# Optimization experiments

Hardware: AMD Instinct MI355X
Metric: run time of the kernel (lower is better)

Reference implementation:

```python
import jax, jax.numpy as jnp
import numpy as np

N = 50000      # nodes
E = 500000     # edges
H = 128        # hidden_channels
P = 1024       # number of (src,dst) link pairs: z==1 and z==2 counts
L = 3          # num_layers
MAXZ = 1000


def setup_inputs() -> dict:
    key = jax.random.key(0)
    ks = jax.random.split(key, 16)
    # z: P src nodes (label 1), P dst nodes (label 2), rest random labels >= 3
    z = jnp.concatenate([
        jnp.ones((P,), jnp.int32),
        jnp.full((P,), 2, jnp.int32),
        jax.random.randint(ks[0], (N - 2 * P,), 3, MAXZ, dtype=jnp.int32),
    ])
    edge_index = jax.random.randint(ks[1], (2, E), 0, N, dtype=jnp.int32)
    batch = jnp.zeros((N,), jnp.int32)  # unused in executed branch
    s = 1.0 / np.sqrt(H)
    z_table = jax.random.normal(ks[2], (MAXZ, H), jnp.float32) * 0.1
    conv_Wl = jax.random.normal(ks[3], (L, H, H), jnp.float32) * s
    conv_bl = jax.random.normal(ks[4], (L, H), jnp.float32) * 0.01
    conv_Wr = jax.random.normal(ks[5], (L, H, H), jnp.float32) * s
    W0 = jax.random.normal(ks[6], (H, H), jnp.float32) * s
    b0 = jax.random.normal(ks[7], (H,), jnp.float32) * 0.01
    W1 = jax.random.normal(ks[8], (H, H), jnp.float32) * s
    b1 = jax.random.normal(ks[9], (H,), jnp.float32) * 0.01
    W2 = jax.random.normal(ks[10], (1, H), jnp.float32) * s
    b2 = jax.random.normal(ks[11], (1,), jnp.float32) * 0.01
    return dict(z=z, edge_index=edge_index, batch=batch, z_table=z_table,
                conv_Wl=conv_Wl, conv_bl=conv_bl, conv_Wr=conv_Wr,
                W0=W0, b0=b0, W1=W1, b1=b1, W2=W2, b2=b2)


def _sage_conv(x, Wl, bl, Wr, src, dst):
    # x: [2, N, H]; mean-aggregate neighbor messages then linear (PyG SAGEConv)
    msgs = x[:, src, :]  # [2, E, H] gather
    agg = jax.vmap(lambda m: jax.ops.segment_sum(m, dst, num_segments=N))(msgs)
    deg = jax.ops.segment_sum(jnp.ones((dst.shape[0],), x.dtype), dst, num_segments=N)
    agg = agg / jnp.maximum(deg, 1.0)[None, :, None]
    return agg @ Wl.T + bl + x @ Wr.T  # lin_l(mean) + bias + lin_r(x)


def reference(z, edge_index, batch, z_table, conv_Wl, conv_bl, conv_Wr,
              W0, b0, W1, b1, W2, b2):
    src, dst = edge_index[0], edge_index[1]
    # ([[1],[2]] == z).long() -> [2, N] in {0,1}; embed -> [2, N, H]
    lbl = (jnp.arange(1, 3, dtype=z.dtype)[:, None] == z[None, :]).astype(jnp.int32)
    x = z_table[lbl]
    for i in range(L - 1):
        x = jax.nn.relu(_sage_conv(x, conv_Wl[i], conv_bl[i], conv_Wr[i], src, dst))
    x = _sage_conv(x, conv_Wl[L - 1], conv_bl[L - 1], conv_Wr[L - 1], src, dst)
    h = jax.nn.relu(x @ W0.T + b0).sum(axis=0)  # [N, H]
    src_idx = jnp.nonzero(z == 1, size=P)[0]
    dst_idx = jnp.nonzero(z == 2, size=P)[0]
    p = h[src_idx] * h[dst_idx]                 # [P, H]
    return jax.nn.relu(p @ W1.T + b1) @ W2.T + b2  # [P, 1]
```

## Files before the change

kernel.cpp:

```cpp
#include <hip/hip_runtime.h>
#include <stdint.h>

#define HH 128
typedef unsigned long long ull;
typedef unsigned short u16;

__device__ __forceinline__ ull shfl_up64(ull v, int d) {
  unsigned lo = (unsigned)__shfl_up((int)(unsigned)(v & 0xffffffffULL), d);
  unsigned hi = (unsigned)__shfl_up((int)(unsigned)(v >> 32), d);
  return ((ull)hi << 32) | (ull)lo;
}
__device__ __forceinline__ ull shfl_down64(ull v, int d) {
  unsigned lo = (unsigned)__shfl_down((int)(unsigned)(v & 0xffffffffULL), d);
  unsigned hi = (unsigned)__shfl_down((int)(unsigned)(v >> 32), d);
  return ((ull)hi << 32) | (ull)lo;
}

__global__ __launch_bounds__(256) void k_ytab(
    const float* __restrict__ zt, const float* __restrict__ Wl0,
    const float* __restrict__ Wr0, const float* __restrict__ Wl2,
    const float* __restrict__ Wr2, const float* __restrict__ bl0,
    const float* __restrict__ bl1, float* __restrict__ y_l,
    float* __restrict__ y_rb, float* __restrict__ vecs_g,
    const int* __restrict__ z, int N, ull* __restrict__ cnt64,
    int* __restrict__ mark) {
  __shared__ float ztS[2][HH];
  __shared__ float vS[4][HH];
  __shared__ float xS[16][HH];
  int t = threadIdx.x;
  {
    int gid = blockIdx.x * 256 + t;
    int nthr = gridDim.x * 256;
    for (int n = gid; n < N; n += nthr) {
      cnt64[n] = 0ULL;
      mark[n] = (z[n] <= 2) ? 1 : 0;
    }
  }
  ztS[t >> 7][t & 127] = zt[t];
  __syncthreads();
#pragma unroll
  for (int rep = 0; rep < 2; rep++) {
    int idx = t + rep * 256;
    int m = idx >> 7, j = idx & 127;
    const float* W = (m < 2) ? Wl0 : Wr0;
    const float* zrow = ztS[m & 1];
    float acc = 0.f;
    for (int k = 0; k < HH; k++) acc = fmaf(zrow[k], W[j * HH + k], acc);
    vS[m][j] = acc;
  }
  __syncthreads();
  if (blockIdx.x == 0) {
    vecs_g[t] = vS[t >> 7][t & 127];
    vecs_g[256 + t] = vS[2 + (t >> 7)][t & 127];
  }
  int v0 = blockIdx.x * 16;
#pragma unroll
  for (int rep = 0; rep < 8; rep++) {
    int idx = t + rep * 256;
    int r = idx >> 7, j = idx & 127;
    int v = v0 + r;
    int d = v >> 4, cnt = (v >> 1) & 7, sel = v & 1;
    float invd = 1.0f / (float)max(d, 1);
    float u1 = (float)cnt * invd, u0 = (float)(d - cnt) * invd;
    xS[r][j] = fmaxf(fmaf(u0, vS[0][j], fmaf(u1, vS[1][j], bl0[j] + vS[2 + sel][j])), 0.f);
  }
  __syncthreads();
  int j = t & 127, rh = t >> 7;
  float al[8], ar[8];
#pragma unroll
  for (int q = 0; q < 8; q++) { al[q] = 0.f; ar[q] = 0.f; }
  for (int k = 0; k < HH; k++) {
    float wl = Wl2[j * HH + k], wr = Wr2[j * HH + k];
#pragma unroll
    for (int q = 0; q < 8; q++) {
      float x = xS[rh * 8 + q][k];
      al[q] = fmaf(x, wl, al[q]);
      ar[q] = fmaf(x, wr, ar[q]);
    }
  }
  float bb = bl1[j];
#pragma unroll
  for (int q = 0; q < 8; q++) {
    int v = v0 + rh * 8 + q;
    y_l[((size_t)v << 7) + j] = al[q];
    y_rb[((size_t)v << 7) + j] = ar[q] + bb;
  }
}

__global__ void k_edge(const int* __restrict__ z, const int* __restrict__ src,
                       const int* __restrict__ dst, int E,
                       ull* __restrict__ cnt64, int* __restrict__ mark,
                       int* __restrict__ pos) {
  int tid = blockIdx.x * blockDim.x + threadIdx.x;
  int stride = gridDim.x * blockDim.x;
  for (int e = tid; e < E; e += stride) {
    int s = src[e], d = dst[e];
    int zs = z[s];
    ull val = 1ULL | ((ull)(zs == 1) << 20) | ((ull)(zs == 2) << 40);
    ull old = atomicAdd(&cnt64[d], val);
    pos[e] = (int)(old & 0xFFFFF);
    if (z[d] <= 2) mark[s] = 1;
  }
}

__global__ void k_scan1(const ull* __restrict__ cnt64, const int* __restrict__ mark,
                        const int* __restrict__ z, int N,
                        ull* __restrict__ locout, ull* __restrict__ partials) {
  __shared__ ull wsum[4];
  int t = threadIdx.x, b = blockIdx.x;
  int base = b * 1024 + t * 4;
  ull l[4]; ull s = 0;
  for (int i = 0; i < 4; i++) {
    int idx = base + i; ull v = 0;
    if (idx < N) {
      int zz = z[idx];
      v = (cnt64[idx] & 0xFFFFFULL) | ((ull)mark[idx] << 20)
        | ((ull)(zz == 1) << 40) | ((ull)(zz == 2) << 52);
    }
    l[i] = s; s += v;
  }
  int lane = t & 63, wid = t >> 6;
  ull vi = s;
  for (int d2 = 1; d2 < 64; d2 <<= 1) { ull o = shfl_up64(vi, d2); if (lane >= d2) vi += o; }
  if (lane == 63) wsum[wid] = vi;
  __syncthreads();
  ull woff = 0;
  for (int w = 0; w < wid; w++) woff += wsum[w];
  ull thrbase = woff + vi - s;
  for (int i = 0; i < 4; i++) {
    int idx = base + i;
    if (idx < N) locout[idx] = thrbase + l[i];
  }
  if (t == 255) partials[b] = woff + vi;
}

__global__ __launch_bounds__(256) void k_post(const ull* __restrict__ locout, const ull* __restrict__ partials,
                       const int* __restrict__ z, const int* __restrict__ mark,
                       const ull* __restrict__ cnt64,
                       int N, int P, int* __restrict__ rowptr, int* __restrict__ mlist,
                       int* __restrict__ minv, int* __restrict__ plist,
                       int* __restrict__ Rm, int4* __restrict__ pack,
                       u16* __restrict__ keyN) {
  __shared__ ull base_s;
  int t = threadIdx.x;
  if (t < 64) {
    int need = blockIdx.x >> 2;
    ull v = (t < need) ? partials[t] : 0ULL;
    for (int o = 32; o > 0; o >>= 1) v += shfl_down64(v, o);
    if (t == 0) base_s = v;
  }
  __syncthreads();
  int n = blockIdx.x * 256 + t;
  if (n >= N) return;
  ull s = locout[n] + base_s;
  int rp = (int)(s & 0xFFFFF);
  int mp = (int)((s >> 20) & 0xFFFFF);
  int r1 = (int)((s >> 40) & 0xFFF);
  int r2 = (int)(s >> 52);
  rowptr[n] = rp;
  int mk = mark[n];
  if (mk) { mlist[mp] = n; minv[n] = mp; }
  int zz = z[n];
  if (zz == 1) plist[r1] = n;
  else if (zz == 2) plist[P + r2] = n;
  ull cv = cnt64[n];
  int dd = (int)(cv & 0xFFFFF), c1 = (int)((cv >> 20) & 0xFFFFF), c2 = (int)((cv >> 40) & 0xFFFFF);
  pack[n] = make_int4(dd, c1, c2, zz);
  int wcls = (zz == 1) ? 1 : ((zz == 2) ? 2 : 0);
  u16 key;
  if (dd < 64 && c1 < 8 && c2 < 8) key = (u16)(dd | (c1 << 6) | (c2 << 9) | (wcls << 12));
  else key = 0x8000;
  keyN[n] = key;
  if (n == N - 1) *Rm = mp + mk;
}

__global__ void k_csrk(const int* __restrict__ src, const int* __restrict__ dst, int E,
                       const int* __restrict__ rowptr, const int* __restrict__ pos,
                       const u16* __restrict__ keyN, ull* __restrict__ csrk) {
  int e = blockIdx.x * blockDim.x + threadIdx.x;
  if (e >= E) return;
  int d = dst[e], s = src[e];
  csrk[rowptr[d] + pos[e]] = (ull)(unsigned)s | ((ull)keyN[s] << 32);
}

__device__ __noinline__ float4 yrow_fb(const float* __restrict__ vecs,
    const float* __restrict__ bl0, const float* __restrict__ Wm,
    int j4, int d, int cnt, int sel) {
  float invd = 1.0f / (float)max(d, 1);
  float u1 = (float)cnt * invd, u0 = (float)(d - cnt) * invd;
  const float* Rv = vecs + (2 + sel) * HH;
  float4 acc = make_float4(0, 0, 0, 0);
  for (int k = 0; k < HH; k++) {
    float x = fmaxf(fmaf(u0, vecs[k], fmaf(u1, vecs[HH + k], bl0[k] + Rv[k])), 0.f);
    acc.x = fmaf(x, Wm[(j4 + 0) * HH + k], acc.x);
    acc.y = fmaf(x, Wm[(j4 + 1) * HH + k], acc.y);
    acc.z = fmaf(x, Wm[(j4 + 2) * HH + k], acc.z);
    acc.w = fmaf(x, Wm[(j4 + 3) * HH + k], acc.w);
  }
  return acc;
}

__device__ __forceinline__ float4 yl_fetch(ull cv, int ch, int chsel, int j4,
    const float* __restrict__ y_l, const int4* __restrict__ pack,
    const float* __restrict__ vecs, const float* __restrict__ bl0,
    const float* __restrict__ Wl2) {
  int key = (int)(cv >> 32);
  if (key & 0x8000) {
    int s = (int)(cv & 0xFFFFFFFFULL);
    int4 p = pack[s];
    int cc = ch ? p.z : p.y;
    int sel = (p.w == chsel) ? 1 : 0;
    return yrow_fb(vecs, bl0, Wl2, j4, p.x, cc, sel);
  }
  int cc = (key >> (6 + 3 * ch)) & 7;
  int sel = (((key >> 12) & 3) == chsel) ? 1 : 0;
  int row = ((key & 63) << 4) + (cc << 1) + sel;
  return *(const float4*)(y_l + ((size_t)row << 7) + j4);
}

__global__ __launch_bounds__(256) void k_agg2Y(const int4* __restrict__ pack,
    const ull* __restrict__ csrk, const float* __restrict__ y_l,
    const float* __restrict__ y_rb, const float* __restrict__ vecs,
    const float* __restrict__ bl0, const float* __restrict__ bl1,
    const float* __restrict__ Wl2, const float* __restrict__ Wr2,
    const int* __restrict__ rowptr, const int* __restrict__ mlist,
    const int* __restrict__ Rdev, float* __restrict__ x2c) {
  int gt = blockIdx.x * blockDim.x + threadIdx.x;
  int w = gt >> 6, lane = gt & 63;
  int nw = (gridDim.x * blockDim.x) >> 6;
  int T = *Rdev;
  int ch = lane >> 5, j4 = (lane & 31) * 4;
  int chsel = ch + 1;
  for (int task = w; task < T; task += nw) {
    int n = mlist[task];
    int4 pn = pack[n];
    int beg = rowptr[n], d = pn.x;
    float4 acc = make_float4(0, 0, 0, 0);
    int i = 0;
    for (; i + 4 <= d; i += 4) {
      ull c0 = csrk[beg + i], c1 = csrk[beg + i + 1];
      ull c2 = csrk[beg + i + 2], c3 = csrk[beg + i + 3];
      float4 v0 = yl_fetch(c0, ch, chsel, j4, y_l, pack, vecs, bl0, Wl2);
      float4 v1 = yl_fetch(c1, ch, chsel, j4, y_l, pack, vecs, bl0, Wl2);
      float4 v2 = yl_fetch(c2, ch, chsel, j4, y_l, pack, vecs, bl0, Wl2);
      float4 v3 = yl_fetch(c3, ch, chsel, j4, y_l, pack, vecs, bl0, Wl2);
      acc.x += v0.x + v1.x + v2.x + v3.x;
      acc.y += v0.y + v1.y + v2.y + v3.y;
      acc.z += v0.z + v1.z + v2.z + v3.z;
      acc.w += v0.w + v1.w + v2.w + v3.w;
    }
    for (; i < d; i++) {
      float4 v0 = yl_fetch(csrk[beg + i], ch, chsel, j4, y_l, pack, vecs, bl0, Wl2);
      acc.x += v0.x; acc.y += v0.y; acc.z += v0.z; acc.w += v0.w;
    }
    float inv = 1.0f / (float)max(d, 1);
    int ccn = ch ? pn.z : pn.y;
    int seln = (pn.w == chsel) ? 1 : 0;
    float4 yr;
    if (pn.x < 64 && ccn < 8) {
      yr = *(const float4*)(y_rb + ((size_t)(((pn.x << 3) + ccn) * 2 + seln) << 7) + j4);
    } else {
      yr = yrow_fb(vecs, bl0, Wr2, j4, pn.x, ccn, seln);
      yr.x += bl1[j4]; yr.y += bl1[j4 + 1]; yr.z += bl1[j4 + 2]; yr.w += bl1[j4 + 3];
    }
    float4 o;
    o.x = fmaxf(fmaf(acc.x, inv, yr.x), 0.f);
    o.y = fmaxf(fmaf(acc.y, inv, yr.y), 0.f);
    o.z = fmaxf(fmaf(acc.z, inv, yr.z), 0.f);
    o.w = fmaxf(fmaf(acc.w, inv, yr.w), 0.f);
    *(float4*)(x2c + (size_t)task * 256 + ch * HH + j4) = o;
  }
}

#define G3 8
__global__ __launch_bounds__(256) void k_aggL3F(const float* __restrict__ x2c,
    const ull* __restrict__ csrk, const int* __restrict__ rowptr,
    const int4* __restrict__ pack, const int* __restrict__ plist,
    const int* __restrict__ minv, const float* __restrict__ Wl3,
    const float* __restrict__ Wr3, const float* __restrict__ W0,
    const float* __restrict__ bl2, const float* __restrict__ b0,
    float* __restrict__ tmp0) {
  __shared__ float aS[G3][256];
  __shared__ float xS[G3][256];
  __shared__ float x3S[G3][256];
  int t = threadIdx.x;
  int i0 = blockIdx.x * G3;
  for (int g = 0; g < G3; g++) {
    int i = i0 + g;
    int n = plist[i];
    int beg = rowptr[n], d = pack[n].x;
    float acc = 0.f;
    int k = 0;
    for (; k + 4 <= d; k += 4) {
      int m0 = minv[(int)(csrk[beg + k] & 0xFFFFFFFFULL)];
      int m1 = minv[(int)(csrk[beg + k + 1] & 0xFFFFFFFFULL)];
      int m2 = minv[(int)(csrk[beg + k + 2] & 0xFFFFFFFFULL)];
      int m3 = minv[(int)(csrk[beg + k + 3] & 0xFFFFFFFFULL)];
      acc += x2c[(size_t)m0 * 256 + t] + x2c[(size_t)m1 * 256 + t]
           + x2c[(size_t)m2 * 256 + t] + x2c[(size_t)m3 * 256 + t];
    }
    for (; k < d; k++)
      acc += x2c[(size_t)minv[(int)(csrk[beg + k] & 0xFFFFFFFFULL)] * 256 + t];
    aS[g][t] = acc / (float)max(d, 1);
    xS[g][t] = x2c[(size_t)minv[n] * 256 + t];
  }
  __syncthreads();
  {
    int c = t >> 7, j = t & 127;
    float acc[G3];
#pragma unroll
    for (int g = 0; g < G3; g++) acc[g] = bl2[j];
    for (int k = 0; k < HH; k++) {
      float wl = Wl3[j * HH + k], wr = Wr3[j * HH + k];
#pragma unroll
      for (int g = 0; g < G3; g++)
        acc[g] = fmaf(aS[g][c * HH + k], wl, fmaf(xS[g][c * HH + k], wr, acc[g]));
    }
#pragma unroll
    for (int g = 0; g < G3; g++) x3S[g][t] = acc[g];
  }
  __syncthreads();
  {
    int c = t >> 7, j = t & 127;
    float acc[G3];
#pragma unroll
    for (int g = 0; g < G3; g++) acc[g] = b0[j];
    for (int k = 0; k < HH; k++) {
      float w0 = W0[j * HH + k];
#pragma unroll
      for (int g = 0; g < G3; g++) acc[g] = fmaf(x3S[g][c * HH + k], w0, acc[g]);
    }
#pragma unroll
    for (int g = 0; g < G3; g++)
      tmp0[(size_t)(2 * (i0 + g) + c) * HH + j] = fmaxf(acc[g], 0.f);
  }
}

__global__ __launch_bounds__(256) void k_finalP(const float* __restrict__ tmp0,
    const float* __restrict__ W1, const float* __restrict__ b1,
    const float* __restrict__ W2, const float* __restrict__ b2,
    int P, float* __restrict__ out) {
  __shared__ float pS[2][HH];
  __shared__ float wred[4];
  int t = threadIdx.x;
  int half = t >> 7, j = t & 127;
  int i = blockIdx.x * 2 + half;
  float hs = tmp0[(size_t)(2 * i) * HH + j] + tmp0[(size_t)(2 * i + 1) * HH + j];
  float hd = tmp0[(size_t)(2 * (i + P)) * HH + j] + tmp0[(size_t)(2 * (i + P) + 1) * HH + j];
  pS[half][j] = hs * hd;
  __syncthreads();
  float acc = b1[j];
#pragma unroll 8
  for (int k = 0; k < HH; k++) acc = fmaf(pS[half][k], W1[j * HH + k], acc);
  float v = fmaxf(acc, 0.f) * W2[j];
  for (int off = 32; off > 0; off >>= 1) v += __shfl_down(v, off);
  int wid = t >> 6, lane = t & 63;
  if (lane == 0) wred[wid] = v;
  __syncthreads();
  if (t == 0) out[i] = wred[0] + wred[1] + b2[0];
  else if (t == 128) out[i] = wred[2] + wred[3] + b2[0];
}

extern "C" void kernel_launch(void* const* d_in, const int* in_sizes, int n_in,
                              void* d_out, int out_size, void* d_ws, size_t ws_size,
                              hipStream_t stream) {
  const int* z = (const int*)d_in[0];
  const int* ei = (const int*)d_in[1];
  const float* z_table = (const float*)d_in[3];
  const float* conv_Wl = (const float*)d_in[4];
  const float* conv_bl = (const float*)d_in[5];
  const float* conv_Wr = (const float*)d_in[6];
  const float* W0 = (const float*)d_in[7];
  const float* b0 = (const float*)d_in[8];
  const float* W1 = (const float*)d_in[9];
  const float* b1 = (const float*)d_in[10];
  const float* W2 = (const float*)d_in[11];
  const float* b2 = (const float*)d_in[12];
  float* out = (float*)d_out;

  int N = in_sizes[0];
  int E = in_sizes[1] / 2;
  int P = out_size;
  int P2 = 2 * P;
  const int* srcA = ei;
  const int* dstA = ei + E;

  char* basep = (char*)d_ws;
  size_t off = 0;
  auto alloc = [&](size_t bytes) -> char* {
    off = (off + 255) & ~(size_t)255;
    char* pp = basep + off; off += bytes; return pp;
  };
  float* y_l   = (float*)alloc((size_t)1024 * HH * 4);
  float* y_rb  = (float*)alloc((size_t)1024 * HH * 4);
  float* vecs  = (float*)alloc((size_t)4 * HH * 4);
  float* x2c   = (float*)alloc((size_t)N * 256 * 4);
  float* tmp0  = (float*)alloc((size_t)2 * P2 * HH * 4);
  ull*   cnt64 = (ull*)alloc((size_t)N * 8);
  int*   mark  = (int*)alloc((size_t)N * 4);
  int*   pos   = (int*)alloc((size_t)E * 4);
  int*   rowptr= (int*)alloc((size_t)N * 4);
  int*   mlist = (int*)alloc((size_t)N * 4);
  int*   minv  = (int*)alloc((size_t)N * 4);
  int*   plist = (int*)alloc((size_t)P2 * 4);
  ull*   csrk  = (ull*)alloc((size_t)E * 8);
  ull*   locout= (ull*)alloc((size_t)N * 8);
  ull*   partials = (ull*)alloc(256 * 8);
  int*   Rm_dev = (int*)alloc(256);
  u16*   keyN  = (u16*)alloc((size_t)N * 2);
  int4*  pack  = (int4*)alloc((size_t)N * 16);
  (void)ws_size; (void)n_in;

  k_ytab<<<64, 256, 0, stream>>>(z_table, conv_Wl, conv_Wr,
                                 conv_Wl + HH * HH, conv_Wr + HH * HH,
                                 conv_bl, conv_bl + HH, y_l, y_rb, vecs,
                                 z, N, cnt64, mark);
  k_edge<<<1024, 256, 0, stream>>>(z, srcA, dstA, E, cnt64, mark, pos);
  int nb = (N + 1023) / 1024;
  k_scan1<<<nb, 256, 0, stream>>>(cnt64, mark, z, N, locout, partials);
  k_post<<<(N + 255) / 256, 256, 0, stream>>>(locout, partials, z, mark, cnt64, N, P,
                                              rowptr, mlist, minv, plist, Rm_dev, pack, keyN);
  k_csrk<<<(E + 255) / 256, 256, 0, stream>>>(srcA, dstA, E, rowptr, pos, keyN, csrk);
  k_agg2Y<<<2048, 256, 0, stream>>>(pack, csrk, y_l, y_rb, vecs, conv_bl, conv_bl + HH,
                                    conv_Wl + HH * HH, conv_Wr + HH * HH,
                                    rowptr, mlist, Rm_dev, x2c);
  k_aggL3F<<<P2 / G3, 256, 0, stream>>>(x2c, csrk, rowptr, pack, plist, minv,
                                        conv_Wl + 2 * HH * HH, conv_Wr + 2 * HH * HH,
                                        W0, conv_bl + 2 * HH, b0, tmp0);
  k_finalP<<<P / 2, 256, 0, stream>>>(tmp0, W1, b1, W2, b2, P, out);
}
```

Before: 148.1 us.

## Split layer-3 aggregation into wavefront-parallel gather kernel and LDS-tiled GEMM

The fused layer-3 kernel is split in two. A new gather kernel assigns one 64-lane wavefront per link node, using float4 loads, and writes the mean aggregate to a new buffer. A separate GEMM kernel handles 4 nodes per block and stages Wl3/Wr3/W0 through transposed, padded shared-memory tiles instead of strided global reads. The aim is more parallelism in the gather and coalesced weight reuse, at the cost of an extra launch and a round trip of the aggregate through global memory.

```diff
diff --git a/kernel.cpp b/kernel.cpp
--- a/kernel.cpp
+++ b/kernel.cpp
@@ -272,68 +272,116 @@
   }
 }
 
-#define G3 8
-__global__ __launch_bounds__(256) void k_aggL3F(const float* __restrict__ x2c,
+__global__ __launch_bounds__(256) void k_agg3(const float* __restrict__ x2c,
     const ull* __restrict__ csrk, const int* __restrict__ rowptr,
     const int4* __restrict__ pack, const int* __restrict__ plist,
-    const int* __restrict__ minv, const float* __restrict__ Wl3,
+    const int* __restrict__ minv, int T, float* __restrict__ aggp) {
+  int gt = blockIdx.x * blockDim.x + threadIdx.x;
+  int w = gt >> 6, lane = gt & 63;
+  int nw = (gridDim.x * blockDim.x) >> 6;
+  int j4 = lane * 4;
+  for (int task = w; task < T; task += nw) {
+    int n = plist[task];
+    int beg = rowptr[n], d = pack[n].x;
+    float4 acc = make_float4(0, 0, 0, 0);
+    int i = 0;
+    for (; i + 4 <= d; i += 4) {
+      int m0 = minv[(int)(csrk[beg + i] & 0xFFFFFFFFULL)];
+      int m1 = minv[(int)(csrk[beg + i + 1] & 0xFFFFFFFFULL)];
+      int m2 = minv[(int)(csrk[beg + i + 2] & 0xFFFFFFFFULL)];
+      int m3 = minv[(int)(csrk[beg + i + 3] & 0xFFFFFFFFULL)];
+      float4 v0 = *(const float4*)(x2c + (size_t)m0 * 256 + j4);
+      float4 v1 = *(const float4*)(x2c + (size_t)m1 * 256 + j4);
+      float4 v2 = *(const float4*)(x2c + (size_t)m2 * 256 + j4);
+      float4 v3 = *(const float4*)(x2c + (size_t)m3 * 256 + j4);
+      acc.x += v0.x + v1.x + v2.x + v3.x;
+      acc.y += v0.y + v1.y + v2.y + v3.y;
+      acc.z += v0.z + v1.z + v2.z + v3.z;
+      acc.w += v0.w + v1.w + v2.w + v3.w;
+    }
+    for (; i < d; i++) {
+      int m0 = minv[(int)(csrk[beg + i] & 0xFFFFFFFFULL)];
+      float4 v0 = *(const float4*)(x2c + (size_t)m0 * 256 + j4);
+      acc.x += v0.x; acc.y += v0.y; acc.z += v0.z; acc.w += v0.w;
+    }
+    float inv = 1.0f / (float)max(d, 1);
+    float4 o = make_float4(acc.x * inv, acc.y * inv, acc.z * inv, acc.w * inv);
+    *(float4*)(aggp + (size_t)task * 256 + j4) = o;
+  }
+}
+
+#define G3 4
+__global__ __launch_bounds__(256) void k_gemm3F(const float* __restrict__ aggp,
+    const float* __restrict__ x2c, const float* __restrict__ Wl3,
     const float* __restrict__ Wr3, const float* __restrict__ W0,
     const float* __restrict__ bl2, const float* __restrict__ b0,
+    const int* __restrict__ plist, const int* __restrict__ minv,
     float* __restrict__ tmp0) {
-  __shared__ float aS[G3][256];
-  __shared__ float xS[G3][256];
-  __shared__ float x3S[G3][256];
+  __shared__ float aS[G3][256], xS[G3][256], x3S[G3][256];
+  __shared__ float wAS[32][HH + 1], wBS[32][HH + 1];
   int t = threadIdx.x;
   int i0 = blockIdx.x * G3;
+  int j = t & 127, c = t >> 7;
+#pragma unroll
   for (int g = 0; g < G3; g++) {
     int i = i0 + g;
-    int n = plist[i];
-    int beg = rowptr[n], d = pack[n].x;
-    float acc = 0.f;
-    int k = 0;
-    for (; k + 4 <= d; k += 4) {
-      int m0 = minv[(int)(csrk[beg + k] & 0xFFFFFFFFULL)];
-      int m1 = minv[(int)(csrk[beg + k + 1] & 0xFFFFFFFFULL)];
-      int m2 = minv[(int)(csrk[beg + k + 2] & 0xFFFFFFFFULL)];
-      int m3 = minv[(int)(csrk[beg + k + 3] & 0xFFFFFFFFULL)];
-      acc += x2c[(size_t)m0 * 256 + t] + x2c[(size_t)m1 * 256 + t]
-           + x2c[(size_t)m2 * 256 + t] + x2c[(size_t)m3 * 256 + t];
-    }
-    for (; k < d; k++)
-      acc += x2c[(size_t)minv[(int)(csrk[beg + k] & 0xFFFFFFFFULL)] * 256 + t];
-    aS[g][t] = acc / (float)max(d, 1);
-    xS[g][t] = x2c[(size_t)minv[n] * 256 + t];
-  }
-  __syncthreads();
-  {
-    int c = t >> 7, j = t & 127;
-    float acc[G3];
-#pragma unroll
-    for (int g = 0; g < G3; g++) acc[g] = bl2[j];
-    for (int k = 0; k < HH; k++) {
-      float wl = Wl3[j * HH + k], wr = Wr3[j * HH + k];
+    aS[g][t] = aggp[(size_t)i * 256 + t];
+    xS[g][t] = x2c[(size_t)minv[plist[i]] * 256 + t];
+  }
+  float acc[G3];
+#pragma unroll
+  for (int g = 0; g < G3; g++) acc[g] = bl2[j];
+  int jw = t >> 3;
+  int kk0 = (t & 7) * 4;
+  for (int kt = 0; kt < 4; kt++) {
+    __syncthreads();
+#pragma unroll
+    for (int q = 0; q < 4; q++) {
+      int jj = q * 32 + jw;
+      float4 va = *(const float4*)(Wl3 + (size_t)jj * HH + kt * 32 + kk0);
+      float4 vb = *(const float4*)(Wr3 + (size_t)jj * HH + kt * 32 + kk0);
+      wAS[kk0 + 0][jj] = va.x; wAS[kk0 + 1][jj] = va.y;
+      wAS[kk0 + 2][jj] = va.z; wAS[kk0 + 3][jj] = va.w;
+      wBS[kk0 + 0][jj] = vb.x; wBS[kk0 + 1][jj] = vb.y;
+      wBS[kk0 + 2][jj] = vb.z; wBS[kk0 + 3][jj] = vb.w;
+    }
+    __syncthreads();
+#pragma unroll
+    for (int kk = 0; kk < 32; kk++) {
+      int k = kt * 32 + kk;
+      float wl = wAS[kk][j], wr = wBS[kk][j];
 #pragma unroll
       for (int g = 0; g < G3; g++)
         acc[g] = fmaf(aS[g][c * HH + k], wl, fmaf(xS[g][c * HH + k], wr, acc[g]));
     }
-#pragma unroll
-    for (int g = 0; g < G3; g++) x3S[g][t] = acc[g];
-  }
-  __syncthreads();
-  {
-    int c = t >> 7, j = t & 127;
-    float acc[G3];
-#pragma unroll
-    for (int g = 0; g < G3; g++) acc[g] = b0[j];
-    for (int k = 0; k < HH; k++) {
-      float w0 = W0[j * HH + k];
-#pragma unroll
-      for (int g = 0; g < G3; g++) acc[g] = fmaf(x3S[g][c * HH + k], w0, acc[g]);
-    }
-#pragma unroll
-    for (int g = 0; g < G3; g++)
-      tmp0[(size_t)(2 * (i0 + g) + c) * HH + j] = fmaxf(acc[g], 0.f);
-  }
+  }
+#pragma unroll
+  for (int g = 0; g < G3; g++) x3S[g][t] = acc[g];
+  float acc2[G3];
+#pragma unroll
+  for (int g = 0; g < G3; g++) acc2[g] = b0[j];
+  for (int kt = 0; kt < 4; kt++) {
+    __syncthreads();
+#pragma unroll
+    for (int q = 0; q < 4; q++) {
+      int jj = q * 32 + jw;
+      float4 v0 = *(const float4*)(W0 + (size_t)jj * HH + kt * 32 + kk0);
+      wAS[kk0 + 0][jj] = v0.x; wAS[kk0 + 1][jj] = v0.y;
+      wAS[kk0 + 2][jj] = v0.z; wAS[kk0 + 3][jj] = v0.w;
+    }
+    __syncthreads();
+#pragma unroll
+    for (int kk = 0; kk < 32; kk++) {
+      int k = kt * 32 + kk;
+      float w0v = wAS[kk][j];
+#pragma unroll
+      for (int g = 0; g < G3; g++)
+        acc2[g] = fmaf(x3S[g][c * HH + k], w0v, acc2[g]);
+    }
+  }
+#pragma unroll
+  for (int g = 0; g < G3; g++)
+    tmp0[(size_t)(2 * (i0 + g) + c) * HH + j] = fmaxf(acc2[g], 0.f);
 }
 
 __global__ __launch_bounds__(256) void k_finalP(const float* __restrict__ tmp0,
@@ -395,6 +443,7 @@
   float* y_rb  = (float*)alloc((size_t)1024 * HH * 4);
   float* vecs  = (float*)alloc((size_t)4 * HH * 4);
   float* x2c   = (float*)alloc((size_t)N * 256 * 4);
+  float* aggp  = (float*)alloc((size_t)P2 * 256 * 4);
   float* tmp0  = (float*)alloc((size_t)2 * P2 * HH * 4);
   ull*   cnt64 = (ull*)alloc((size_t)N * 8);
   int*   mark  = (int*)alloc((size_t)N * 4);
@@ -424,8 +473,9 @@
   k_agg2Y<<<2048, 256, 0, stream>>>(pack, csrk, y_l, y_rb, vecs, conv_bl, conv_bl + HH,
                                     conv_Wl + HH * HH, conv_Wr + HH * HH,
                                     rowptr, mlist, Rm_dev, x2c);
-  k_aggL3F<<<P2 / G3, 256, 0, stream>>>(x2c, csrk, rowptr, pack, plist, minv,
-                                        conv_Wl + 2 * HH * HH, conv_Wr + 2 * HH * HH,
-                                        W0, conv_bl + 2 * HH, b0, tmp0);
+  k_agg3<<<512, 256, 0, stream>>>(x2c, csrk, rowptr, pack, plist, minv, P2, aggp);
+  k_gemm3F<<<P2 / G3, 256, 0, stream>>>(aggp, x2c, conv_Wl + 2 * HH * HH,
+                                        conv_Wr + 2 * HH * HH, W0,
+                                        conv_bl + 2 * HH, b0, plist, minv, tmp0);
   k_finalP<<<P / 2, 256, 0, stream>>>(tmp0, W1, b1, W2, b2, P, out);
 }
```

Result: faster. 132.7 us (-10.4%).
